# Kernel optimization log

Hardware: AMD Instinct MI355X
Metric: run time of the kernel (lower is better)

The kernel has to match this reference:

```python
import jax, jax.numpy as jnp
import numpy as np

B, T, F = 1024, 512, 32
H, E, L = 128, 16, 2
N_TICKERS = 5000


def _gru_layer(x_seq, W_ih, W_hh, b_ih, b_hh):
    # x_seq: [B, T, I]; W_ih: [3H, I]; W_hh: [3H, H]. PyTorch gate order: r, z, n.
    gx = jnp.einsum('bti,gi->btg', x_seq, W_ih) + b_ih  # [B, T, 3H]

    def step(h, gx_t):
        gh = h @ W_hh.T + b_hh                     # [B, 3H]
        r = jax.nn.sigmoid(gx_t[:, :H] + gh[:, :H])
        z = jax.nn.sigmoid(gx_t[:, H:2 * H] + gh[:, H:2 * H])
        n = jnp.tanh(gx_t[:, 2 * H:] + r * gh[:, 2 * H:])
        h_new = (1.0 - z) * n + z * h
        return h_new, h_new

    h0 = jnp.zeros((x_seq.shape[0], H), dtype=x_seq.dtype)
    _, hs = jax.lax.scan(step, h0, jnp.swapaxes(gx, 0, 1))  # hs: [T, B, H]
    return jnp.swapaxes(hs, 0, 1)                            # [B, T, H]


def setup_inputs() -> dict:
    key = jax.random.key(0)
    ks = jax.random.split(key, 16)
    s_in0 = 1.0 / np.sqrt(H)
    inp = {
        'x': jax.random.normal(ks[0], (B, T, F), dtype=jnp.float32),
        'ticker_ids': jax.random.randint(ks[1], (B,), 0, N_TICKERS),
        'embed': jax.random.normal(ks[2], (N_TICKERS, E), dtype=jnp.float32),
        # GRU layer 0 (input size F+E=48)
        'W_ih0': jax.random.uniform(ks[3], (3 * H, F + E), minval=-s_in0, maxval=s_in0),
        'W_hh0': jax.random.uniform(ks[4], (3 * H, H), minval=-s_in0, maxval=s_in0),
        'b_ih0': jax.random.uniform(ks[5], (3 * H,), minval=-s_in0, maxval=s_in0),
        'b_hh0': jax.random.uniform(ks[6], (3 * H,), minval=-s_in0, maxval=s_in0),
        # GRU layer 1 (input size H)
        'W_ih1': jax.random.uniform(ks[7], (3 * H, H), minval=-s_in0, maxval=s_in0),
        'W_hh1': jax.random.uniform(ks[8], (3 * H, H), minval=-s_in0, maxval=s_in0),
        'b_ih1': jax.random.uniform(ks[9], (3 * H,), minval=-s_in0, maxval=s_in0),
        'b_hh1': jax.random.uniform(ks[10], (3 * H,), minval=-s_in0, maxval=s_in0),
        # head: Linear(H,H) -> ReLU -> Linear(H,1)
        'head_w1': jax.random.uniform(ks[11], (H, H), minval=-s_in0, maxval=s_in0),
        'head_b1': jax.random.uniform(ks[12], (H,), minval=-s_in0, maxval=s_in0),
        'head_w2': jax.random.uniform(ks[13], (1, H), minval=-s_in0, maxval=s_in0),
        'head_b2': jax.random.uniform(ks[14], (1,), minval=-s_in0, maxval=s_in0),
    }
    return inp


def reference(x, ticker_ids, embed, W_ih0, W_hh0, b_ih0, b_hh0,
              W_ih1, W_hh1, b_ih1, b_hh1, head_w1, head_b1, head_w2, head_b2):
    emb = embed[ticker_ids]                                  # [B, E]
    emb_seq = jnp.broadcast_to(emb[:, None, :], (x.shape[0], x.shape[1], emb.shape[-1]))
    xcat = jnp.concatenate([x, emb_seq], axis=-1)            # [B, T, F+E]
    h = _gru_layer(xcat, W_ih0, W_hh0, b_ih0, b_hh0)         # [B, T, H]
    h = _gru_layer(h, W_ih1, W_hh1, b_ih1, b_hh1)            # [B, T, H]
    last = h[:, -1, :]                                       # [B, H]
    hid = jax.nn.relu(last @ head_w1.T + head_b1)            # dropout inactive at eval
    y = (hid @ head_w2.T + head_b2)[:, 0]                    # [B]
    return y
```

## Files before the change

### kernel.cpp

```cpp
#include <hip/hip_runtime.h>

constexpr int kB  = 1024;
constexpr int kT  = 512;
constexpr int kF  = 32;
constexpr int kE  = 16;
constexpr int kH  = 128;
constexpr int kMB = 16;
constexpr int kNMB = kB / kMB;
constexpr int kTc = 32;
constexpr int kNCh = kT / kTc;
constexpr int kTg = kTc / 2;
constexpr size_t kH0Str = (size_t)kB * kTc * kH;
constexpr size_t kSlots = (size_t)kNMB * kTc * 512;

typedef __attribute__((ext_vector_type(8))) _Float16 f16x8;
typedef __attribute__((ext_vector_type(4))) _Float16 f16x4;
typedef __attribute__((ext_vector_type(4))) float    f32x4;

#define MFMA16(a,b,c) __builtin_amdgcn_mfma_f32_16x16x32_f16(a,b,c,0,0,0)

__device__ __forceinline__ float sigm_hw(float x){
    float e = __builtin_amdgcn_exp2f(-1.442695041f * x);
    return __builtin_amdgcn_rcpf(1.0f + e);
}
__device__ __forceinline__ float tanh_hw(float x){
    float e = __builtin_amdgcn_exp2f(-2.885390082f * x);
    return fmaf(2.0f, __builtin_amdgcn_rcpf(1.0f + e), -1.0f);
}
__device__ __forceinline__ void splitF(float v, _Float16 &hi, _Float16 &lo){
    hi = (_Float16)v;
    lo = (_Float16)(v - (float)hi);
}
__device__ __forceinline__ f16x8 loadW8(const float* __restrict__ p){
    f16x8 r;
#pragma unroll
    for (int j=0;j<8;j++) r[j] = (_Float16)p[j];
    return r;
}
__device__ __forceinline__ unsigned short f2u(_Float16 h){ return __builtin_bit_cast(unsigned short, h); }
__device__ __forceinline__ _Float16 u2f(unsigned short u){ return __builtin_bit_cast(_Float16, u); }
__device__ __forceinline__ unsigned pack2(float a, float b){
    return (unsigned)f2u((_Float16)a) | ((unsigned)f2u((_Float16)b) << 16);
}
__device__ __forceinline__ void bar_lds(){
    asm volatile("s_waitcnt lgkmcnt(0)\n\ts_barrier" ::: "memory");
}

struct SRec {
    alignas(16) _Float16 hH[2][16][136];
    alignas(16) _Float16 hL[2][16][136];
    alignas(16) _Float16 xHp[2][16][40];
    alignas(16) _Float16 xLp[2][16][40];
    alignas(16) float hf[16][132];
    alignas(16) float hf2[16][132];
};
struct SGem {
    alignas(16) _Float16 aH[2][16][136];
    alignas(16) _Float16 aL[2][16][136];
};
union SU { SRec r; SGem g; };

__attribute__((amdgpu_waves_per_eu(2, 2)))
__global__ void __launch_bounds__(512) rnn_fused(
    const float* __restrict__ x, const int* __restrict__ tick,
    const float* __restrict__ embed,
    const float* __restrict__ Wih0, const float* __restrict__ Whh0,
    const float* __restrict__ bih0, const float* __restrict__ bhh0,
    const float* __restrict__ Wih1, const float* __restrict__ bih1,
    const float* __restrict__ Whh1, const float* __restrict__ bhh1,
    const float* __restrict__ hw1, const float* __restrict__ hb1,
    const float* __restrict__ hw2, const float* __restrict__ hb2,
    unsigned* __restrict__ h0seq, unsigned* __restrict__ gxA,
    unsigned* __restrict__ gxB, float* __restrict__ h1state,
    float* __restrict__ out, int c)
{
    __shared__ SU sm;
    const int tid = threadIdx.x;
    const int w = tid >> 6, l = tid & 63, lm = l & 15, lq = l >> 4;
    const int i = 16*w + lm;
    const int cls[3] = { i, 128 + i, 256 + i };

    if (blockIdx.x < 64) {
        if (c >= kNCh) return;
        SRec &S = sm.r;
        const int mb = blockIdx.x, b0 = mb * kMB;
        unsigned* h0w = h0seq + (size_t)(c & 1) * kH0Str;

        f16x8 wv[3][4], xw[3];
#pragma unroll
        for (int T=0; T<3; T++){
#pragma unroll
            for (int kt=0; kt<4; kt++)
                wv[T][kt] = loadW8(Whh0 + (size_t)cls[T]*kH + kt*32 + lq*8);
            xw[T] = loadW8(Wih0 + (size_t)cls[T]*48 + lq*8);
        }
        float rIni[4], zIni[4], nxIni[4], nhIni;
        {
            float br = bih0[cls[0]] + bhh0[cls[0]];
            float bz = bih0[cls[1]] + bhh0[cls[1]];
            float bn = bih0[cls[2]];
            nhIni = bhh0[cls[2]];
            const float* w0 = Wih0 + (size_t)cls[0]*48 + 32;
            const float* w1 = Wih0 + (size_t)cls[1]*48 + 32;
            const float* w2 = Wih0 + (size_t)cls[2]*48 + 32;
#pragma unroll
            for (int q=0; q<4; q++){
                const float* ep = embed + (size_t)tick[b0 + lq*4 + q] * kE;
                float s0=0.f, s1=0.f, s2=0.f;
#pragma unroll
                for (int e=0; e<kE; e++){
                    float ev = ep[e];
                    s0 = fmaf(ev, w0[e], s0);
                    s1 = fmaf(ev, w1[e], s1);
                    s2 = fmaf(ev, w2[e], s2);
                }
                rIni[q]=br+s0; zIni[q]=bz+s1; nxIni[q]=bn+s2;
            }
        }
        float hreg[4];
        if (c == 0){
#pragma unroll
            for (int q=0;q<4;q++){
                hreg[q]=0.f;
                S.hH[0][lq*4+q][i]=(_Float16)0.f;
                S.hL[0][lq*4+q][i]=(_Float16)0.f;
            }
        } else {
            const unsigned* h0p = h0seq + (size_t)((c-1) & 1) * kH0Str;
#pragma unroll
            for (int q=0;q<4;q++){
                unsigned u = h0p[((size_t)(mb*kTc + kTc-1)*16 + lq*4+q)*kH + i];
                _Float16 hh = u2f((unsigned short)(u>>16)), hl = u2f((unsigned short)u);
                hreg[q] = (float)hh + (float)hl;
                S.hH[0][lq*4+q][i]=hh; S.hL[0][lq*4+q][i]=hl;
            }
        }
        const int xm = tid >> 5, xk = tid & 31;
        const size_t xbase = (size_t)(b0+xm)*kT*kF + xk;
        {
            _Float16 a2,b2; splitF(x[xbase + (size_t)(c*kTc)*kF], a2, b2);
            S.xHp[0][xm][xk]=a2; S.xLp[0][xm][xk]=b2;
        }
        int t1 = c*kTc + 1; if (t1 > kT-1) t1 = kT-1;
        float xnext = x[xbase + (size_t)t1*kF];
        bar_lds();

        int buf = 0;
        for (int tc=0; tc<kTc; tc++){
            const int nb = buf ^ 1;
            f16x8 aHf[4], aLf[4];
#pragma unroll
            for (int kt=0;kt<4;kt++){
                aHf[kt] = *(const f16x8*)&S.hH[buf][lm][kt*32 + lq*8];
                aLf[kt] = *(const f16x8*)&S.hL[buf][lm][kt*32 + lq*8];
            }
            f16x8 xvH = *(const f16x8*)&S.xHp[buf][lm][lq*8];
            f16x8 xvL = *(const f16x8*)&S.xLp[buf][lm][lq*8];
            f32x4 aR ={rIni[0],rIni[1],rIni[2],rIni[3]};
            f32x4 aZ ={zIni[0],zIni[1],zIni[2],zIni[3]};
            f32x4 aNX={nxIni[0],nxIni[1],nxIni[2],nxIni[3]};
            f32x4 aNH={nhIni,nhIni,nhIni,nhIni};
#pragma unroll
            for (int kt=0;kt<4;kt++){
                aR =MFMA16(aHf[kt],wv[0][kt],aR);  aR =MFMA16(aLf[kt],wv[0][kt],aR);
                aZ =MFMA16(aHf[kt],wv[1][kt],aZ);  aZ =MFMA16(aLf[kt],wv[1][kt],aZ);
                aNH=MFMA16(aHf[kt],wv[2][kt],aNH); aNH=MFMA16(aLf[kt],wv[2][kt],aNH);
            }
            aR =MFMA16(xvH,xw[0],aR);  aR =MFMA16(xvL,xw[0],aR);
            aZ =MFMA16(xvH,xw[1],aZ);  aZ =MFMA16(xvL,xw[1],aZ);
            aNX=MFMA16(xvH,xw[2],aNX); aNX=MFMA16(xvL,xw[2],aNX);
            unsigned pk[4];
#pragma unroll
            for (int q=0;q<4;q++){
                float r = sigm_hw(aR[q]);
                float z = sigm_hw(aZ[q]);
                float n = tanh_hw(fmaf(r, aNH[q], aNX[q]));
                float h = fmaf(z, hreg[q]-n, n);
                hreg[q] = h;
                _Float16 hh,hl; splitF(h,hh,hl);
                S.hH[nb][lq*4+q][i]=hh;
                S.hL[nb][lq*4+q][i]=hl;
                pk[q] = ((unsigned)f2u(hh)<<16) | f2u(hl);
            }
#pragma unroll
            for (int q=0;q<4;q++)
                h0w[((size_t)(mb*kTc + tc)*16 + lq*4+q)*kH + i] = pk[q];
            {
                _Float16 a2,b2; splitF(xnext,a2,b2);
                S.xHp[nb][xm][xk]=a2; S.xLp[nb][xm][xk]=b2;
                int tn = c*kTc + tc + 2; if (tn > kT-1) tn = kT-1;
                xnext = x[xbase + (size_t)tn*kF];
            }
            bar_lds();
            buf = nb;
        }
    } else if (blockIdx.x < 192) {
        const int g = c - 1;
        if (g < 0 || g >= kNCh) return;
        SGem &S = sm.g;
        const int bid = blockIdx.x - 64;
        const int mb = bid >> 1, t0 = (bid & 1) * kTg;
        const unsigned* h0r = h0seq + (size_t)(g & 1) * kH0Str;
        unsigned* gA = gxA + (size_t)(g & 1) * kSlots * 4;
        unsigned* gB = gxB + (size_t)(g & 1) * kSlots * 2;

        f16x8 wv[3][4]; float bI[3];
#pragma unroll
        for (int T=0; T<3; T++){
#pragma unroll
            for (int kt=0; kt<4; kt++)
                wv[T][kt] = loadW8(Wih1 + (size_t)cls[T]*kH + kt*32 + lq*8);
            bI[T] = bih1[cls[T]];
        }
        const int sr = tid >> 5, sq = tid & 31;
        auto ld = [&](int t){
            return *(const uint4*)(h0r + ((size_t)(mb*kTc + t)*16 + sr)*kH + 4*sq);
        };
        auto stage = [&](int bf, uint4 u){
            f16x4 vh = { u2f((unsigned short)(u.x>>16)), u2f((unsigned short)(u.y>>16)),
                         u2f((unsigned short)(u.z>>16)), u2f((unsigned short)(u.w>>16)) };
            f16x4 vl = { u2f((unsigned short)u.x), u2f((unsigned short)u.y),
                         u2f((unsigned short)u.z), u2f((unsigned short)u.w) };
            *(f16x4*)&S.aH[bf][sr][4*sq] = vh;
            *(f16x4*)&S.aL[bf][sr][4*sq] = vl;
        };
        stage(0, ld(t0));
        uint4 nxt = ld(t0 + 1);
        bar_lds();
        for (int tt=0; tt<kTg; tt++){
            const int t = t0 + tt, bf = tt & 1;
            f16x8 fH[4], fL[4];
#pragma unroll
            for (int kt=0;kt<4;kt++){
                fH[kt] = *(const f16x8*)&S.aH[bf][lm][kt*32 + lq*8];
                fL[kt] = *(const f16x8*)&S.aL[bf][lm][kt*32 + lq*8];
            }
            if (tt+1 < kTg) stage(bf^1, nxt);
            if (tt+2 < kTg) nxt = ld(t0 + tt + 2);
            f32x4 aR = {bI[0],bI[0],bI[0],bI[0]};
            f32x4 aZ = {bI[1],bI[1],bI[1],bI[1]};
            f32x4 aN = {bI[2],bI[2],bI[2],bI[2]};
#pragma unroll
            for (int kt=0;kt<4;kt++){
                aR=MFMA16(fH[kt],wv[0][kt],aR); aR=MFMA16(fL[kt],wv[0][kt],aR);
                aZ=MFMA16(fH[kt],wv[1][kt],aZ); aZ=MFMA16(fL[kt],wv[1][kt],aZ);
                aN=MFMA16(fH[kt],wv[2][kt],aN); aN=MFMA16(fL[kt],wv[2][kt],aN);
            }
            const size_t slot = ((size_t)mb*kTc + t)*512 + tid;
            *(uint4*)(gA + slot*4) = make_uint4(pack2(aR[0],aR[1]), pack2(aR[2],aR[3]),
                                                pack2(aZ[0],aZ[1]), pack2(aZ[2],aZ[3]));
            *(uint2*)(gB + slot*2) = make_uint2(pack2(aN[0],aN[1]), pack2(aN[2],aN[3]));
            bar_lds();
        }
    } else {
        const int e0 = c - 2;
        if (e0 < 0 || e0 >= kNCh) return;
        SRec &S = sm.r;
        const int mb = blockIdx.x - 192, b0 = mb * kMB;
        const unsigned* gA = gxA + (size_t)(e0 & 1) * kSlots * 4;
        const unsigned* gB = gxB + (size_t)(e0 & 1) * kSlots * 2;

        f16x8 wv[3][4];
#pragma unroll
        for (int T=0; T<3; T++)
#pragma unroll
            for (int kt=0; kt<4; kt++)
                wv[T][kt] = loadW8(Whh1 + (size_t)cls[T]*kH + kt*32 + lq*8);
        const float br = bhh1[cls[0]], bz = bhh1[cls[1]], bn = bhh1[cls[2]];

        float hreg[4];
        if (e0 == 0){
#pragma unroll
            for (int q=0;q<4;q++){
                hreg[q]=0.f;
                S.hH[0][lq*4+q][i]=(_Float16)0.f;
                S.hL[0][lq*4+q][i]=(_Float16)0.f;
            }
        } else {
#pragma unroll
            for (int q=0;q<4;q++){
                float h = h1state[(size_t)(b0 + lq*4+q)*kH + i];
                hreg[q]=h;
                _Float16 hh,hl; splitF(h,hh,hl);
                S.hH[0][lq*4+q][i]=hh; S.hL[0][lq*4+q][i]=hl;
            }
        }
        const size_t base = (size_t)mb*kTc*512 + tid;
        uint4 g4c = *(const uint4*)(gA + base*4);
        uint2 g2c = *(const uint2*)(gB + base*2);
        uint4 g4n = *(const uint4*)(gA + (base + 512)*4);
        uint2 g2n = *(const uint2*)(gB + (base + 512)*2);
        bar_lds();

        int buf = 0;
        for (int tc=0; tc<kTc; tc++){
            const int nb = buf ^ 1;
            f16x8 aHf[4], aLf[4];
#pragma unroll
            for (int kt=0;kt<4;kt++){
                aHf[kt] = *(const f16x8*)&S.hH[buf][lm][kt*32 + lq*8];
                aLf[kt] = *(const f16x8*)&S.hL[buf][lm][kt*32 + lq*8];
            }
            f32x4 aR={br,br,br,br}, aZ={bz,bz,bz,bz}, aNH={bn,bn,bn,bn};
#pragma unroll
            for (int kt=0;kt<4;kt++){
                aR =MFMA16(aHf[kt],wv[0][kt],aR);  aR =MFMA16(aLf[kt],wv[0][kt],aR);
                aZ =MFMA16(aHf[kt],wv[1][kt],aZ);  aZ =MFMA16(aLf[kt],wv[1][kt],aZ);
                aNH=MFMA16(aHf[kt],wv[2][kt],aNH); aNH=MFMA16(aLf[kt],wv[2][kt],aNH);
            }
            const float rx[4] = { (float)u2f((unsigned short)g4c.x), (float)u2f((unsigned short)(g4c.x>>16)),
                                  (float)u2f((unsigned short)g4c.y), (float)u2f((unsigned short)(g4c.y>>16)) };
            const float zx[4] = { (float)u2f((unsigned short)g4c.z), (float)u2f((unsigned short)(g4c.z>>16)),
                                  (float)u2f((unsigned short)g4c.w), (float)u2f((unsigned short)(g4c.w>>16)) };
            const float nx[4] = { (float)u2f((unsigned short)g2c.x), (float)u2f((unsigned short)(g2c.x>>16)),
                                  (float)u2f((unsigned short)g2c.y), (float)u2f((unsigned short)(g2c.y>>16)) };
#pragma unroll
            for (int q=0;q<4;q++){
                float r = sigm_hw(aR[q] + rx[q]);
                float z = sigm_hw(aZ[q] + zx[q]);
                float n = tanh_hw(fmaf(r, aNH[q], nx[q]));
                float h = fmaf(z, hreg[q]-n, n);
                hreg[q] = h;
                _Float16 hh,hl; splitF(h,hh,hl);
                S.hH[nb][lq*4+q][i]=hh;
                S.hL[nb][lq*4+q][i]=hl;
            }
            g4c = g4n; g2c = g2n;
            int tn = tc + 2; if (tn > kTc-1) tn = kTc-1;
            g4n = *(const uint4*)(gA + (base + (size_t)tn*512)*4);
            g2n = *(const uint2*)(gB + (base + (size_t)tn*512)*2);
            bar_lds();
            buf = nb;
        }
#pragma unroll
        for (int q=0;q<4;q++)
            h1state[(size_t)(b0 + lq*4+q)*kH + i] = hreg[q];
        if (e0 == kNCh-1){
#pragma unroll
            for (int q=0;q<4;q++) S.hf[lq*4+q][i] = hreg[q];
            __syncthreads();
            const int hm = tid >> 5, i0 = (tid & 31) * 4;
#pragma unroll
            for (int e=0;e<4;e++){
                const float* wr = hw1 + (size_t)(i0+e)*kH;
                float s = hb1[i0+e];
                for (int k2=0;k2<kH;k2++) s = fmaf(wr[k2], S.hf[hm][k2], s);
                S.hf2[hm][i0+e] = fmaxf(s, 0.f);
            }
            __syncthreads();
            if (tid < kMB){
                float s = hb2[0];
                for (int k2=0;k2<kH;k2++) s = fmaf(S.hf2[tid][k2], hw2[k2], s);
                out[b0 + tid] = s;
            }
        }
    }
}

extern "C" void kernel_launch(void* const* d_in, const int* in_sizes, int n_in,
                              void* d_out, int out_size, void* d_ws, size_t ws_size,
                              hipStream_t stream)
{
    const float* x     = (const float*)d_in[0];
    const int*   tick  = (const int*)d_in[1];
    const float* embed = (const float*)d_in[2];
    const float* Wih0  = (const float*)d_in[3];
    const float* Whh0  = (const float*)d_in[4];
    const float* bih0  = (const float*)d_in[5];
    const float* bhh0  = (const float*)d_in[6];
    const float* Wih1  = (const float*)d_in[7];
    const float* Whh1  = (const float*)d_in[8];
    const float* bih1  = (const float*)d_in[9];
    const float* bhh1  = (const float*)d_in[10];
    const float* hw1   = (const float*)d_in[11];
    const float* hb1   = (const float*)d_in[12];
    const float* hw2   = (const float*)d_in[13];
    const float* hb2   = (const float*)d_in[14];
    float* out = (float*)d_out;

    unsigned* h0seq = (unsigned*)d_ws;
    unsigned* gxA   = h0seq + 2*kH0Str;
    unsigned* gxB   = gxA + 2*kSlots*4;
    float*  h1state = (float*)(gxB + 2*kSlots*2);

    for (int c = 0; c <= kNCh + 1; c++){
        rnn_fused<<<256, 512, 0, stream>>>(x, tick, embed,
            Wih0, Whh0, bih0, bhh0, Wih1, bih1, Whh1, bhh1,
            hw1, hb1, hw2, hb2, h0seq, gxA, gxB, h1state, out, c);
    }
}
```

Measured before the change: 1.227 ms.

## Stream x tiles into LDS via async global_load_lds with swizzled layout

Replaces the per-step register prefetch and f16 split of the x input in the layer-0 recurrence with bulk asynchronous global-to-LDS loads of 8-timestep fp32 tiles, double-buffered and XOR-swizzled to avoid bank conflicts. The hi/lo split now happens on read, inside the step loop. This removes per-step global load latency and LDS stores from the serial critical path. It adds splitF work per step and explicit vmcnt waits at the refill boundaries, and the x buffer now shares LDS with the head scratch through a union.

```diff
diff --git a/kernel.cpp b/kernel.cpp
--- a/kernel.cpp
+++ b/kernel.cpp
@@ -45,14 +45,22 @@
 __device__ __forceinline__ void bar_lds(){
     asm volatile("s_waitcnt lgkmcnt(0)\n\ts_barrier" ::: "memory");
 }
+__device__ __forceinline__ void gload_lds4(const float* __restrict__ gp, unsigned* lp){
+    __builtin_amdgcn_global_load_lds(
+        (const __attribute__((address_space(1))) void*)gp,
+        (__attribute__((address_space(3))) void*)lp, 4, 0, 0);
+}
 
 struct SRec {
     alignas(16) _Float16 hH[2][16][136];
     alignas(16) _Float16 hL[2][16][136];
-    alignas(16) _Float16 xHp[2][16][40];
-    alignas(16) _Float16 xLp[2][16][40];
-    alignas(16) float hf[16][132];
-    alignas(16) float hf2[16][132];
+    union {
+        alignas(16) unsigned xf[2][8][512];
+        struct {
+            alignas(16) float hf[16][132];
+            alignas(16) float hf2[16][132];
+        } h;
+    } u;
 };
 struct SGem {
     alignas(16) _Float16 aH[2][16][136];
@@ -135,15 +143,21 @@
                 S.hH[0][lq*4+q][i]=hh; S.hL[0][lq*4+q][i]=hl;
             }
         }
-        const int xm = tid >> 5, xk = tid & 31;
-        const size_t xbase = (size_t)(b0+xm)*kT*kF + xk;
-        {
-            _Float16 a2,b2; splitF(x[xbase + (size_t)(c*kTc)*kF], a2, b2);
-            S.xHp[0][xm][xk]=a2; S.xLp[0][xm][xk]=b2;
-        }
-        int t1 = c*kTc + 1; if (t1 > kT-1) t1 = kT-1;
-        float xnext = x[xbase + (size_t)t1*kF];
-        bar_lds();
+        const int m7 = lm & 7;
+        const int xrd0 = lm*32 + ((lq*8    ) ^ (m7 << 2));
+        const int xrd1 = lm*32 + ((lq*8 + 4) ^ (m7 << 2));
+        auto refill = [&](int half, int tb){
+#pragma unroll
+            for (int j=0;j<8;j++){
+                const int mm = j*2 + (l >> 5);
+                const int kk = (l & 31) ^ ((mm & 7) << 2);
+                const float* gp = x + (size_t)(b0+mm)*kT*kF + (size_t)(tb + w)*kF + kk;
+                gload_lds4(gp, &S.u.xf[half][w][j*64]);
+            }
+        };
+        refill(0, c*kTc);
+        refill(1, c*kTc + 8);
+        __syncthreads();
 
         int buf = 0;
         for (int tc=0; tc<kTc; tc++){
@@ -154,8 +168,21 @@
                 aHf[kt] = *(const f16x8*)&S.hH[buf][lm][kt*32 + lq*8];
                 aLf[kt] = *(const f16x8*)&S.hL[buf][lm][kt*32 + lq*8];
             }
-            f16x8 xvH = *(const f16x8*)&S.xHp[buf][lm][lq*8];
-            f16x8 xvL = *(const f16x8*)&S.xLp[buf][lm][lq*8];
+            const unsigned* xp = &S.u.xf[(tc>>3)&1][tc&7][0];
+            const uint4 xa = *(const uint4*)(xp + xrd0);
+            const uint4 xb = *(const uint4*)(xp + xrd1);
+            f16x8 xvH, xvL;
+            {
+                const unsigned xs[8] = { xa.x, xa.y, xa.z, xa.w, xb.x, xb.y, xb.z, xb.w };
+#pragma unroll
+                for (int j=0;j<8;j++){
+                    _Float16 hh,hl;
+                    splitF(__builtin_bit_cast(float, xs[j]), hh, hl);
+                    xvH[j]=hh; xvL[j]=hl;
+                }
+            }
+            if (tc == 8)  refill(0, c*kTc + 16);
+            if (tc == 16) refill(1, c*kTc + 24);
             f32x4 aR ={rIni[0],rIni[1],rIni[2],rIni[3]};
             f32x4 aZ ={zIni[0],zIni[1],zIni[2],zIni[3]};
             f32x4 aNX={nxIni[0],nxIni[1],nxIni[2],nxIni[3]};
@@ -185,12 +212,8 @@
 #pragma unroll
             for (int q=0;q<4;q++)
                 h0w[((size_t)(mb*kTc + tc)*16 + lq*4+q)*kH + i] = pk[q];
-            {
-                _Float16 a2,b2; splitF(xnext,a2,b2);
-                S.xHp[nb][xm][xk]=a2; S.xLp[nb][xm][xk]=b2;
-                int tn = c*kTc + tc + 2; if (tn > kT-1) tn = kT-1;
-                xnext = x[xbase + (size_t)tn*kF];
-            }
+            if (tc == 15 || tc == 23)
+                asm volatile("s_waitcnt vmcnt(0)" ::: "memory");
             bar_lds();
             buf = nb;
         }
@@ -337,20 +360,20 @@
             h1state[(size_t)(b0 + lq*4+q)*kH + i] = hreg[q];
         if (e0 == kNCh-1){
 #pragma unroll
-            for (int q=0;q<4;q++) S.hf[lq*4+q][i] = hreg[q];
+            for (int q=0;q<4;q++) S.u.h.hf[lq*4+q][i] = hreg[q];
             __syncthreads();
             const int hm = tid >> 5, i0 = (tid & 31) * 4;
 #pragma unroll
             for (int e=0;e<4;e++){
                 const float* wr = hw1 + (size_t)(i0+e)*kH;
                 float s = hb1[i0+e];
-                for (int k2=0;k2<kH;k2++) s = fmaf(wr[k2], S.hf[hm][k2], s);
-                S.hf2[hm][i0+e] = fmaxf(s, 0.f);
+                for (int k2=0;k2<kH;k2++) s = fmaf(wr[k2], S.u.h.hf[hm][k2], s);
+                S.u.h.hf2[hm][i0+e] = fmaxf(s, 0.f);
             }
             __syncthreads();
             if (tid < kMB){
                 float s = hb2[0];
-                for (int k2=0;k2<kH;k2++) s = fmaf(S.hf2[tid][k2], hw2[k2], s);
+                for (int k2=0;k2<kH;k2++) s = fmaf(S.u.h.hf2[tid][k2], hw2[k2], s);
                 out[b0 + tid] = s;
             }
         }
```

Result: slower. 1.328 ms (+8.2%).

## Precompute layer-0 input projection one chunk ahead on GEMM blocks

Applied to the files above, without the earlier changes.

Moves the layer-0 input projection (x and embedding times W_ih0 plus bias) out of the sequential recurrence blocks and into the GEMM block group, which computes it one chunk ahead into a new fp32 double-buffered workspace. The recurrence loop then drops six MFMAs and the x staging through LDS per step, and instead prefetches precomputed gate inputs from global memory. This shortens the serial critical path. In exchange it adds an extra launch (c = -1), extra global traffic for fp32 gate inputs, and a larger workspace.

```diff
diff --git a/kernel.cpp b/kernel.cpp
--- a/kernel.cpp
+++ b/kernel.cpp
@@ -12,6 +12,7 @@
 constexpr int kTg = kTc / 2;
 constexpr size_t kH0Str = (size_t)kB * kTc * kH;
 constexpr size_t kSlots = (size_t)kNMB * kTc * 512;
+constexpr size_t kGx0Str = kSlots * 12;
 
 typedef __attribute__((ext_vector_type(8))) _Float16 f16x8;
 typedef __attribute__((ext_vector_type(4))) _Float16 f16x4;
@@ -42,6 +43,7 @@
 __device__ __forceinline__ unsigned pack2(float a, float b){
     return (unsigned)f2u((_Float16)a) | ((unsigned)f2u((_Float16)b) << 16);
 }
+__device__ __forceinline__ float uf(unsigned u){ return __builtin_bit_cast(float, u); }
 __device__ __forceinline__ void bar_lds(){
     asm volatile("s_waitcnt lgkmcnt(0)\n\ts_barrier" ::: "memory");
 }
@@ -49,8 +51,6 @@
 struct SRec {
     alignas(16) _Float16 hH[2][16][136];
     alignas(16) _Float16 hL[2][16][136];
-    alignas(16) _Float16 xHp[2][16][40];
-    alignas(16) _Float16 xLp[2][16][40];
     alignas(16) float hf[16][132];
     alignas(16) float hf2[16][132];
 };
@@ -72,7 +72,7 @@
     const float* __restrict__ hw2, const float* __restrict__ hb2,
     unsigned* __restrict__ h0seq, unsigned* __restrict__ gxA,
     unsigned* __restrict__ gxB, float* __restrict__ h1state,
-    float* __restrict__ out, int c)
+    unsigned* __restrict__ gx0, float* __restrict__ out, int c)
 {
     __shared__ SU sm;
     const int tid = threadIdx.x;
@@ -81,42 +81,20 @@
     const int cls[3] = { i, 128 + i, 256 + i };
 
     if (blockIdx.x < 64) {
-        if (c >= kNCh) return;
+        if (c < 0 || c >= kNCh) return;
         SRec &S = sm.r;
         const int mb = blockIdx.x, b0 = mb * kMB;
         unsigned* h0w = h0seq + (size_t)(c & 1) * kH0Str;
-
-        f16x8 wv[3][4], xw[3];
-#pragma unroll
-        for (int T=0; T<3; T++){
+        const unsigned* g0 = gx0 + (size_t)(c & 1) * kGx0Str;
+
+        f16x8 wv[3][4];
+#pragma unroll
+        for (int T=0; T<3; T++)
 #pragma unroll
             for (int kt=0; kt<4; kt++)
                 wv[T][kt] = loadW8(Whh0 + (size_t)cls[T]*kH + kt*32 + lq*8);
-            xw[T] = loadW8(Wih0 + (size_t)cls[T]*48 + lq*8);
-        }
-        float rIni[4], zIni[4], nxIni[4], nhIni;
-        {
-            float br = bih0[cls[0]] + bhh0[cls[0]];
-            float bz = bih0[cls[1]] + bhh0[cls[1]];
-            float bn = bih0[cls[2]];
-            nhIni = bhh0[cls[2]];
-            const float* w0 = Wih0 + (size_t)cls[0]*48 + 32;
-            const float* w1 = Wih0 + (size_t)cls[1]*48 + 32;
-            const float* w2 = Wih0 + (size_t)cls[2]*48 + 32;
-#pragma unroll
-            for (int q=0; q<4; q++){
-                const float* ep = embed + (size_t)tick[b0 + lq*4 + q] * kE;
-                float s0=0.f, s1=0.f, s2=0.f;
-#pragma unroll
-                for (int e=0; e<kE; e++){
-                    float ev = ep[e];
-                    s0 = fmaf(ev, w0[e], s0);
-                    s1 = fmaf(ev, w1[e], s1);
-                    s2 = fmaf(ev, w2[e], s2);
-                }
-                rIni[q]=br+s0; zIni[q]=bz+s1; nxIni[q]=bn+s2;
-            }
-        }
+        const float br = bhh0[cls[0]], bz = bhh0[cls[1]], bn = bhh0[cls[2]];
+
         float hreg[4];
         if (c == 0){
 #pragma unroll
@@ -135,14 +113,13 @@
                 S.hH[0][lq*4+q][i]=hh; S.hL[0][lq*4+q][i]=hl;
             }
         }
-        const int xm = tid >> 5, xk = tid & 31;
-        const size_t xbase = (size_t)(b0+xm)*kT*kF + xk;
-        {
-            _Float16 a2,b2; splitF(x[xbase + (size_t)(c*kTc)*kF], a2, b2);
-            S.xHp[0][xm][xk]=a2; S.xLp[0][xm][xk]=b2;
-        }
-        int t1 = c*kTc + 1; if (t1 > kT-1) t1 = kT-1;
-        float xnext = x[xbase + (size_t)t1*kF];
+        const size_t base = (size_t)mb*kTc*512 + tid;
+        uint4 grc = *(const uint4*)(g0 + base*12);
+        uint4 gzc = *(const uint4*)(g0 + base*12 + 4);
+        uint4 gnc = *(const uint4*)(g0 + base*12 + 8);
+        uint4 grn = *(const uint4*)(g0 + (base+512)*12);
+        uint4 gzn = *(const uint4*)(g0 + (base+512)*12 + 4);
+        uint4 gnn = *(const uint4*)(g0 + (base+512)*12 + 8);
         bar_lds();
 
         int buf = 0;
@@ -154,27 +131,22 @@
                 aHf[kt] = *(const f16x8*)&S.hH[buf][lm][kt*32 + lq*8];
                 aLf[kt] = *(const f16x8*)&S.hL[buf][lm][kt*32 + lq*8];
             }
-            f16x8 xvH = *(const f16x8*)&S.xHp[buf][lm][lq*8];
-            f16x8 xvL = *(const f16x8*)&S.xLp[buf][lm][lq*8];
-            f32x4 aR ={rIni[0],rIni[1],rIni[2],rIni[3]};
-            f32x4 aZ ={zIni[0],zIni[1],zIni[2],zIni[3]};
-            f32x4 aNX={nxIni[0],nxIni[1],nxIni[2],nxIni[3]};
-            f32x4 aNH={nhIni,nhIni,nhIni,nhIni};
+            f32x4 aR={br,br,br,br}, aZ={bz,bz,bz,bz}, aNH={bn,bn,bn,bn};
 #pragma unroll
             for (int kt=0;kt<4;kt++){
                 aR =MFMA16(aHf[kt],wv[0][kt],aR);  aR =MFMA16(aLf[kt],wv[0][kt],aR);
                 aZ =MFMA16(aHf[kt],wv[1][kt],aZ);  aZ =MFMA16(aLf[kt],wv[1][kt],aZ);
                 aNH=MFMA16(aHf[kt],wv[2][kt],aNH); aNH=MFMA16(aLf[kt],wv[2][kt],aNH);
             }
-            aR =MFMA16(xvH,xw[0],aR);  aR =MFMA16(xvL,xw[0],aR);
-            aZ =MFMA16(xvH,xw[1],aZ);  aZ =MFMA16(xvL,xw[1],aZ);
-            aNX=MFMA16(xvH,xw[2],aNX); aNX=MFMA16(xvL,xw[2],aNX);
+            const float rx[4] = { uf(grc.x), uf(grc.y), uf(grc.z), uf(grc.w) };
+            const float zx[4] = { uf(gzc.x), uf(gzc.y), uf(gzc.z), uf(gzc.w) };
+            const float nx[4] = { uf(gnc.x), uf(gnc.y), uf(gnc.z), uf(gnc.w) };
             unsigned pk[4];
 #pragma unroll
             for (int q=0;q<4;q++){
-                float r = sigm_hw(aR[q]);
-                float z = sigm_hw(aZ[q]);
-                float n = tanh_hw(fmaf(r, aNH[q], aNX[q]));
+                float r = sigm_hw(aR[q] + rx[q]);
+                float z = sigm_hw(aZ[q] + zx[q]);
+                float n = tanh_hw(fmaf(r, aNH[q], nx[q]));
                 float h = fmaf(z, hreg[q]-n, n);
                 hreg[q] = h;
                 _Float16 hh,hl; splitF(h,hh,hl);
@@ -185,72 +157,124 @@
 #pragma unroll
             for (int q=0;q<4;q++)
                 h0w[((size_t)(mb*kTc + tc)*16 + lq*4+q)*kH + i] = pk[q];
-            {
-                _Float16 a2,b2; splitF(xnext,a2,b2);
-                S.xHp[nb][xm][xk]=a2; S.xLp[nb][xm][xk]=b2;
-                int tn = c*kTc + tc + 2; if (tn > kT-1) tn = kT-1;
-                xnext = x[xbase + (size_t)tn*kF];
-            }
+            grc = grn; gzc = gzn; gnc = gnn;
+            int tn = tc + 2; if (tn > kTc-1) tn = kTc-1;
+            grn = *(const uint4*)(g0 + (base + (size_t)tn*512)*12);
+            gzn = *(const uint4*)(g0 + (base + (size_t)tn*512)*12 + 4);
+            gnn = *(const uint4*)(g0 + (base + (size_t)tn*512)*12 + 8);
             bar_lds();
             buf = nb;
         }
     } else if (blockIdx.x < 192) {
-        const int g = c - 1;
-        if (g < 0 || g >= kNCh) return;
-        SGem &S = sm.g;
         const int bid = blockIdx.x - 64;
         const int mb = bid >> 1, t0 = (bid & 1) * kTg;
-        const unsigned* h0r = h0seq + (size_t)(g & 1) * kH0Str;
-        unsigned* gA = gxA + (size_t)(g & 1) * kSlots * 4;
-        unsigned* gB = gxB + (size_t)(g & 1) * kSlots * 2;
-
-        f16x8 wv[3][4]; float bI[3];
-#pragma unroll
-        for (int T=0; T<3; T++){
-#pragma unroll
-            for (int kt=0; kt<4; kt++)
-                wv[T][kt] = loadW8(Wih1 + (size_t)cls[T]*kH + kt*32 + lq*8);
-            bI[T] = bih1[cls[T]];
-        }
-        const int sr = tid >> 5, sq = tid & 31;
-        auto ld = [&](int t){
-            return *(const uint4*)(h0r + ((size_t)(mb*kTc + t)*16 + sr)*kH + 4*sq);
-        };
-        auto stage = [&](int bf, uint4 u){
-            f16x4 vh = { u2f((unsigned short)(u.x>>16)), u2f((unsigned short)(u.y>>16)),
-                         u2f((unsigned short)(u.z>>16)), u2f((unsigned short)(u.w>>16)) };
-            f16x4 vl = { u2f((unsigned short)u.x), u2f((unsigned short)u.y),
-                         u2f((unsigned short)u.z), u2f((unsigned short)u.w) };
-            *(f16x4*)&S.aH[bf][sr][4*sq] = vh;
-            *(f16x4*)&S.aL[bf][sr][4*sq] = vl;
-        };
-        stage(0, ld(t0));
-        uint4 nxt = ld(t0 + 1);
-        bar_lds();
-        for (int tt=0; tt<kTg; tt++){
-            const int t = t0 + tt, bf = tt & 1;
-            f16x8 fH[4], fL[4];
-#pragma unroll
-            for (int kt=0;kt<4;kt++){
-                fH[kt] = *(const f16x8*)&S.aH[bf][lm][kt*32 + lq*8];
-                fL[kt] = *(const f16x8*)&S.aL[bf][lm][kt*32 + lq*8];
-            }
-            if (tt+1 < kTg) stage(bf^1, nxt);
-            if (tt+2 < kTg) nxt = ld(t0 + tt + 2);
-            f32x4 aR = {bI[0],bI[0],bI[0],bI[0]};
-            f32x4 aZ = {bI[1],bI[1],bI[1],bI[1]};
-            f32x4 aN = {bI[2],bI[2],bI[2],bI[2]};
-#pragma unroll
-            for (int kt=0;kt<4;kt++){
-                aR=MFMA16(fH[kt],wv[0][kt],aR); aR=MFMA16(fL[kt],wv[0][kt],aR);
-                aZ=MFMA16(fH[kt],wv[1][kt],aZ); aZ=MFMA16(fL[kt],wv[1][kt],aZ);
-                aN=MFMA16(fH[kt],wv[2][kt],aN); aN=MFMA16(fL[kt],wv[2][kt],aN);
-            }
-            const size_t slot = ((size_t)mb*kTc + t)*512 + tid;
-            *(uint4*)(gA + slot*4) = make_uint4(pack2(aR[0],aR[1]), pack2(aR[2],aR[3]),
-                                                pack2(aZ[0],aZ[1]), pack2(aZ[2],aZ[3]));
-            *(uint2*)(gB + slot*2) = make_uint2(pack2(aN[0],aN[1]), pack2(aN[2],aN[3]));
+        const int b0 = mb * kMB;
+        const int g = c - 1;
+        if (g >= 0 && g < kNCh) {
+            SGem &S = sm.g;
+            const unsigned* h0r = h0seq + (size_t)(g & 1) * kH0Str;
+            unsigned* gA = gxA + (size_t)(g & 1) * kSlots * 4;
+            unsigned* gB = gxB + (size_t)(g & 1) * kSlots * 2;
+
+            f16x8 wv[3][4]; float bI[3];
+#pragma unroll
+            for (int T=0; T<3; T++){
+#pragma unroll
+                for (int kt=0; kt<4; kt++)
+                    wv[T][kt] = loadW8(Wih1 + (size_t)cls[T]*kH + kt*32 + lq*8);
+                bI[T] = bih1[cls[T]];
+            }
+            const int sr = tid >> 5, sq = tid & 31;
+            auto ld = [&](int t){
+                return *(const uint4*)(h0r + ((size_t)(mb*kTc + t)*16 + sr)*kH + 4*sq);
+            };
+            auto stage = [&](int bf, uint4 u){
+                f16x4 vh = { u2f((unsigned short)(u.x>>16)), u2f((unsigned short)(u.y>>16)),
+                             u2f((unsigned short)(u.z>>16)), u2f((unsigned short)(u.w>>16)) };
+                f16x4 vl = { u2f((unsigned short)u.x), u2f((unsigned short)u.y),
+                             u2f((unsigned short)u.z), u2f((unsigned short)u.w) };
+                *(f16x4*)&S.aH[bf][sr][4*sq] = vh;
+                *(f16x4*)&S.aL[bf][sr][4*sq] = vl;
+            };
+            stage(0, ld(t0));
+            uint4 nxt = ld(t0 + 1);
             bar_lds();
+            for (int tt=0; tt<kTg; tt++){
+                const int t = t0 + tt, bf = tt & 1;
+                f16x8 fH[4], fL[4];
+#pragma unroll
+                for (int kt=0;kt<4;kt++){
+                    fH[kt] = *(const f16x8*)&S.aH[bf][lm][kt*32 + lq*8];
+                    fL[kt] = *(const f16x8*)&S.aL[bf][lm][kt*32 + lq*8];
+                }
+                if (tt+1 < kTg) stage(bf^1, nxt);
+                if (tt+2 < kTg) nxt = ld(t0 + tt + 2);
+                f32x4 aR = {bI[0],bI[0],bI[0],bI[0]};
+                f32x4 aZ = {bI[1],bI[1],bI[1],bI[1]};
+                f32x4 aN = {bI[2],bI[2],bI[2],bI[2]};
+#pragma unroll
+                for (int kt=0;kt<4;kt++){
+                    aR=MFMA16(fH[kt],wv[0][kt],aR); aR=MFMA16(fL[kt],wv[0][kt],aR);
+                    aZ=MFMA16(fH[kt],wv[1][kt],aZ); aZ=MFMA16(fL[kt],wv[1][kt],aZ);
+                    aN=MFMA16(fH[kt],wv[2][kt],aN); aN=MFMA16(fL[kt],wv[2][kt],aN);
+                }
+                const size_t slot = ((size_t)mb*kTc + t)*512 + tid;
+                *(uint4*)(gA + slot*4) = make_uint4(pack2(aR[0],aR[1]), pack2(aR[2],aR[3]),
+                                                    pack2(aZ[0],aZ[1]), pack2(aZ[2],aZ[3]));
+                *(uint2*)(gB + slot*2) = make_uint2(pack2(aN[0],aN[1]), pack2(aN[2],aN[3]));
+                bar_lds();
+            }
+        }
+        const int p = c + 1;
+        if (p >= 0 && p < kNCh) {
+            unsigned* g0w = gx0 + (size_t)(p & 1) * kGx0Str;
+            f16x8 xw[3];
+#pragma unroll
+            for (int T=0; T<3; T++)
+                xw[T] = loadW8(Wih0 + (size_t)cls[T]*48 + lq*8);
+            float ini[3][4];
+            {
+                const float bi0 = bih0[cls[0]], bi1 = bih0[cls[1]], bi2 = bih0[cls[2]];
+                const float* w0 = Wih0 + (size_t)cls[0]*48 + 32;
+                const float* w1 = Wih0 + (size_t)cls[1]*48 + 32;
+                const float* w2 = Wih0 + (size_t)cls[2]*48 + 32;
+#pragma unroll
+                for (int q=0; q<4; q++){
+                    const float* ep = embed + (size_t)tick[b0 + lq*4 + q] * kE;
+                    float s0=0.f, s1=0.f, s2=0.f;
+#pragma unroll
+                    for (int e=0; e<kE; e++){
+                        float ev = ep[e];
+                        s0 = fmaf(ev, w0[e], s0);
+                        s1 = fmaf(ev, w1[e], s1);
+                        s2 = fmaf(ev, w2[e], s2);
+                    }
+                    ini[0][q]=bi0+s0; ini[1][q]=bi1+s1; ini[2][q]=bi2+s2;
+                }
+            }
+            for (int tt=0; tt<kTg; tt++){
+                const int t = t0 + tt;
+                const float* xp = x + (size_t)(b0+lm)*kT*kF + (size_t)(p*kTc + t)*kF + lq*8;
+                const float4 xa = *(const float4*)xp;
+                const float4 xb = *(const float4*)(xp + 4);
+                const float xv[8] = { xa.x, xa.y, xa.z, xa.w, xb.x, xb.y, xb.z, xb.w };
+                f16x8 xH, xL;
+#pragma unroll
+                for (int j=0;j<8;j++){
+                    _Float16 hh,hl; splitF(xv[j],hh,hl);
+                    xH[j]=hh; xL[j]=hl;
+                }
+                f32x4 aR = {ini[0][0],ini[0][1],ini[0][2],ini[0][3]};
+                f32x4 aZ = {ini[1][0],ini[1][1],ini[1][2],ini[1][3]};
+                f32x4 aN = {ini[2][0],ini[2][1],ini[2][2],ini[2][3]};
+                aR=MFMA16(xH,xw[0],aR); aR=MFMA16(xL,xw[0],aR);
+                aZ=MFMA16(xH,xw[1],aZ); aZ=MFMA16(xL,xw[1],aZ);
+                aN=MFMA16(xH,xw[2],aN); aN=MFMA16(xL,xw[2],aN);
+                const size_t slot = ((size_t)mb*kTc + t)*512 + tid;
+                *(uint4*)(g0w + slot*12)     = __builtin_bit_cast(uint4, aR);
+                *(uint4*)(g0w + slot*12 + 4) = __builtin_bit_cast(uint4, aZ);
+                *(uint4*)(g0w + slot*12 + 8) = __builtin_bit_cast(uint4, aN);
+            }
         }
     } else {
         const int e0 = c - 2;
@@ -382,10 +406,11 @@
     unsigned* gxA   = h0seq + 2*kH0Str;
     unsigned* gxB   = gxA + 2*kSlots*4;
     float*  h1state = (float*)(gxB + 2*kSlots*2);
-
-    for (int c = 0; c <= kNCh + 1; c++){
+    unsigned* gx0   = (unsigned*)(h1state + (size_t)kB*kH);
+
+    for (int c = -1; c <= kNCh + 1; c++){
         rnn_fused<<<256, 512, 0, stream>>>(x, tick, embed,
             Wih0, Whh0, bih0, bhh0, Wih1, bih1, Whh1, bhh1,
-            hw1, hb1, hw2, hb2, h0seq, gxA, gxB, h1state, out, c);
+            hw1, hb1, hw2, hb2, h0seq, gxA, gxB, h1state, gx0, out, c);
     }
 }
```

After: 1.077 ms. 12.2% less time.
